# Kernel tuning notes

Hardware: AMD Instinct MI355X
Metric: run time of the kernel (lower is better)

Reference implementation:

```python
import jax, jax.numpy as jnp
import numpy as np

B, T, D = 1, 2048, 1024
H, S, LV = 16, 64, 12   # heads, state_size, num_levels = ceil(log2(T)) + 1
HD = D // H             # head_dim = 64
NEG = -1e30


def _level_matrix(length, num_levels):
    """Hierarchical level of key s w.r.t. query t (level_base=2, WEAK htype).

    level(t,s) = 0 if s == t, else floor(log2(s XOR t)) + 1, which is exactly the
    size-class of the Fenwick/dyadic segment of the prefix [0,t) containing s.
    Computed as the count of powers 2^k <= (s XOR t) to avoid float log.
    """
    t = np.arange(length)
    xor = t[:, None] ^ t[None, :]
    lv = np.zeros((length, length), dtype=np.int32)
    for k in range(num_levels - 1):
        lv += (xor >= (1 << k)).astype(np.int32)
    return jnp.asarray(lv)  # [T, T]


def _forward(x, Wq, Wk, Wv, Wdl, Wdt, Wout, A_log, dt_bias, Lp, ln_g, ln_b):
    Bb, Tt, Dd = x.shape
    Q = (x @ Wq.T).reshape(Bb, Tt, H, S)
    K = (x @ Wk.T).reshape(Bb, Tt, H, S)
    V = (x @ Wv.T).reshape(Bb, Tt, H, HD)
    dl = (x @ Wdl.T).reshape(Bb, Tt, H, LV)

    A = -jnp.exp(A_log)                                  # [H]
    dt = jax.nn.softplus(x @ Wdt.T + dt_bias)            # [B,T,H]
    g = A[None, None, :] * dt                            # [B,T,H]  (negative)
    Lam = jax.nn.softplus(Lp[None, None] * dl)           # [B,T,H,LV] lambda per level

    # Mamba2/SSD decay: M[t,s] = exp(sum_{i=s+1..t} g_i), causal
    cg = jnp.cumsum(g, axis=1)                           # [B,T,H]
    diff = cg[:, :, None, :] - cg[:, None, :, :]         # [B,T,S,H]
    tri = np.tril(np.ones((Tt, Tt), dtype=bool))
    decay = jnp.exp(jnp.where(tri[None, :, :, None], diff, NEG))  # [B,T,S,H]

    # hierarchical lambda gate: lam_ts[b,t,h,s] = Lam[b,t,h, level(t,s)]
    levels = _level_matrix(Tt, LV)                       # [T,S] int32
    lam_ts = jnp.take_along_axis(
        Lam[:, :, :, None, :], levels[None, :, None, :, None], axis=-1
    )[..., 0]                                            # [B,T,H,S]

    scores = jnp.einsum('bthd,bshd->bhts', Q, K) * (S ** -0.5)   # [B,H,T,S]
    Wmat = scores * jnp.transpose(decay, (0, 3, 1, 2)) * jnp.transpose(lam_ts, (0, 2, 1, 3))
    Y = jnp.einsum('bhts,bshd->bthd', Wmat, V).reshape(Bb, Tt, H * HD)

    o = Y @ Wout.T + x                                   # out_proj + residual
    mu = o.mean(-1, keepdims=True)
    var = ((o - mu) ** 2).mean(-1, keepdims=True)
    return (o - mu) * jax.lax.rsqrt(var + 1e-5) * ln_g + ln_b


def setup_inputs() -> dict:
    ks = jax.random.split(jax.random.key(0), 8)
    n = jax.random.normal
    w = 0.02
    return {
        'x': n(ks[0], (B, T, D), jnp.float32),
        'Wq': n(ks[1], (H * S, D), jnp.float32) * w,
        'Wk': n(ks[2], (H * S, D), jnp.float32) * w,
        'Wv': n(ks[3], (H * HD, D), jnp.float32) * w,
        'Wdl': n(ks[4], (H * LV, D), jnp.float32) * w,
        'Wdt': n(ks[5], (H, D), jnp.float32) * w,
        'Wout': n(ks[6], (D, H * HD), jnp.float32) * w,
        'A_log': jnp.log(jnp.arange(1, H + 1, dtype=jnp.float32)),
        'dt_bias': n(ks[7], (H,), jnp.float32),
        'Lp': jnp.ones((H, LV), jnp.float32),
        'ln_g': jnp.ones((D,), jnp.float32),
        'ln_b': jnp.zeros((D,), jnp.float32),
    }


def reference(x, Wq, Wk, Wv, Wdl, Wdt, Wout, A_log, dt_bias, Lp, ln_g, ln_b):
    return _forward(x, Wq, Wk, Wv, Wdl, Wdt, Wout, A_log, dt_bias, Lp, ln_g, ln_b)
```

## Files before the change

### kernel.cpp

```cpp
#include <hip/hip_runtime.h>
#include <math.h>

#define Tn 2048
#define Dn 1024
#define Hn 16
#define Sn 64
#define LVn 12
#define HDn 64
#define NQKV 3328

typedef short short8 __attribute__((ext_vector_type(8)));
typedef unsigned short ushortv8 __attribute__((ext_vector_type(8)));
typedef float floatx4 __attribute__((ext_vector_type(4)));

__device__ __forceinline__ float softplus_f(float z) {
  return (z > 0.f) ? (z + log1pf(expf(-z))) : log1pf(expf(z));
}

__device__ __forceinline__ unsigned short f2bf(float f) {
  union { float f; unsigned u; } v; v.f = f;
  unsigned r = v.u + 0x7FFF + ((v.u >> 16) & 1);
  return (unsigned short)(r >> 16);
}

__device__ __forceinline__ void cvt8(const float* s, unsigned short* d) {
  const float4 u0 = *(const float4*)s;
  const float4 u1 = *(const float4*)(s + 4);
  ushortv8 o;
  o[0] = f2bf(u0.x); o[1] = f2bf(u0.y); o[2] = f2bf(u0.z); o[3] = f2bf(u0.w);
  o[4] = f2bf(u1.x); o[5] = f2bf(u1.y); o[6] = f2bf(u1.z); o[7] = f2bf(u1.w);
  *(ushortv8*)d = o;
}

__device__ __forceinline__ void gld16(const void* g, void* l) {
  __builtin_amdgcn_global_load_lds(
      (const __attribute__((address_space(1))) unsigned int*)g,
      (__attribute__((address_space(3))) unsigned int*)l, 16, 0, 0);
}

__global__ __launch_bounds__(256) void cvtdt_k(
    const float* __restrict__ x, const float* __restrict__ Wq,
    const float* __restrict__ Wk, const float* __restrict__ Wv,
    const float* __restrict__ Wdl, const float* __restrict__ Wout,
    const float* __restrict__ Wdt, const float* __restrict__ A_log,
    const float* __restrict__ dt_bias,
    unsigned short* __restrict__ xb, unsigned short* __restrict__ wcat,
    unsigned short* __restrict__ wob, float* __restrict__ g) {
  const int chunk = blockIdx.x;
  const int tid = threadIdx.x;
  if (chunk < 3200) {
    const int eo = tid * 8;
    if (chunk < 1024) {
      const int e = chunk * 2048 + eo;
      cvt8(&x[e], &xb[e]);
    } else if (chunk < 2688) {
      const int e = (chunk - 1024) * 2048 + eo;
      const int row = e >> 10, col = e & 1023;
      if (row < 1024)       cvt8(&Wq[(size_t)row * 1024 + col], &wcat[e]);
      else if (row < 2048)  cvt8(&Wk[(size_t)(row - 1024) * 1024 + col], &wcat[e]);
      else if (row < 3072)  cvt8(&Wv[(size_t)(row - 2048) * 1024 + col], &wcat[e]);
      else if (row < 3264)  cvt8(&Wdl[(size_t)(row - 3072) * 1024 + col], &wcat[e]);
      else                  *(ushortv8*)&wcat[e] = (ushortv8)0;
    } else {
      const int e = (chunk - 2688) * 2048 + eo;
      cvt8(&Wout[e], &wob[e]);
    }
  } else {
    const int t = chunk - 3200;
    __shared__ float xs[Dn];
    ((float4*)xs)[tid] = ((const float4*)&x[(size_t)t * Dn])[tid];
    __syncthreads();
    const int h = tid >> 4, j = tid & 15;
    const float4* xr = (const float4*)&xs[j * 64];
    const float4* wr = (const float4*)&Wdt[h * Dn + j * 64];
    float acc = 0.f;
#pragma unroll
    for (int u = 0; u < 16; ++u) {
      const int up = (u + j) & 15;
      const float4 a = xr[up], b = wr[up];
      acc += a.x * b.x + a.y * b.y + a.z * b.z + a.w * b.w;
    }
#pragma unroll
    for (int st = 1; st < 16; st <<= 1) acc += __shfl_xor(acc, st);
    if (j == 0) {
      const float dtv = softplus_f(acc + dt_bias[h]);
      g[t * Hn + h] = -expf(A_log[h]) * dtv;
    }
  }
}

__global__ __launch_bounds__(256) void mfma_gemm_k(
    const unsigned short* __restrict__ A, const unsigned short* __restrict__ B,
    unsigned short* __restrict__ Cb, float* __restrict__ Cf,
    int by_scan, const float* __restrict__ g, double* __restrict__ cg) {
  __shared__ __attribute__((aligned(16))) unsigned short pool[32768];
  const int tid = threadIdx.x;
  if ((int)blockIdx.y == by_scan) {
    const int h = blockIdx.x;
    if (h >= Hn) return;
    double* ls = (double*)pool;
    double v[8];
    double run = 0.0;
#pragma unroll
    for (int i = 0; i < 8; ++i) {
      run += (double)g[(tid * 8 + i) * Hn + h];
      v[i] = run;
    }
    ls[tid] = run;
    __syncthreads();
    for (int off = 1; off < 256; off <<= 1) {
      double add = (tid >= off) ? ls[tid - off] : 0.0;
      __syncthreads();
      ls[tid] += add;
      __syncthreads();
    }
    const double excl = ls[tid] - run;
#pragma unroll
    for (int i = 0; i < 8; ++i) cg[(tid * 8 + i) * Hn + h] = excl + v[i];
    return;
  }
  unsigned short* lA = pool;
  unsigned short* lB = pool + 16384;
  const int bm = blockIdx.x * 128, bn = blockIdx.y * 128;
  const int lane = tid & 63, wave = tid >> 6;
  const int wm = wave >> 1, wn = wave & 1;
  const int l16 = lane & 15, lk = lane >> 4;
  const int sr = tid >> 2, sc = (tid & 3) * 8;
  floatx4 acc[4][4] = {};
  for (int k0 = 0; k0 < Dn; k0 += 128) {
    __syncthreads();
#pragma unroll
    for (int q = 0; q < 4; ++q) {
      gld16(&A[(size_t)(bm + sr) * Dn + k0 + q * 32 + sc],      &lA[q * 4096 + tid * 8]);
      gld16(&A[(size_t)(bm + 64 + sr) * Dn + k0 + q * 32 + sc], &lA[q * 4096 + 2048 + tid * 8]);
      gld16(&B[(size_t)(bn + sr) * Dn + k0 + q * 32 + sc],      &lB[q * 4096 + tid * 8]);
      gld16(&B[(size_t)(bn + 64 + sr) * Dn + k0 + q * 32 + sc], &lB[q * 4096 + 2048 + tid * 8]);
    }
    __syncthreads();
#pragma unroll
    for (int hh = 0; hh < 4; ++hh) {
      short8 a[4], b[4];
#pragma unroll
      for (int mf = 0; mf < 4; ++mf)
        a[mf] = *(const short8*)&lA[hh * 4096 + (wm * 64 + mf * 16 + l16) * 32 + lk * 8];
#pragma unroll
      for (int nf = 0; nf < 4; ++nf)
        b[nf] = *(const short8*)&lB[hh * 4096 + (wn * 64 + nf * 16 + l16) * 32 + lk * 8];
#pragma unroll
      for (int mf = 0; mf < 4; ++mf)
#pragma unroll
        for (int nf = 0; nf < 4; ++nf)
          acc[mf][nf] = __builtin_amdgcn_mfma_f32_16x16x32_bf16(
              a[mf], b[nf], acc[mf][nf], 0, 0, 0);
    }
  }
  if (bn < 3072) {
    unsigned short (*ctile)[136] = (unsigned short(*)[136])pool;
#pragma unroll
    for (int hh = 0; hh < 2; ++hh) {
      __syncthreads();
      if (wm == hh) {
#pragma unroll
        for (int mf = 0; mf < 4; ++mf)
#pragma unroll
          for (int nf = 0; nf < 4; ++nf)
#pragma unroll
            for (int r = 0; r < 4; ++r)
              ctile[mf * 16 + lk * 4 + r][wn * 64 + nf * 16 + l16] =
                  f2bf(acc[mf][nf][r]);
      }
      __syncthreads();
      const int rr = tid >> 4, cc = (tid & 15) * 8;
#pragma unroll
      for (int j = 0; j < 4; ++j) {
        const int row = rr + j * 16;
        *(ushortv8*)&Cb[(size_t)(bm + hh * 64 + row) * 3072 + bn + cc] =
            *(const ushortv8*)&ctile[row][cc];
      }
    }
    return;
  }
#pragma unroll
  for (int mf = 0; mf < 4; ++mf) {
#pragma unroll
    for (int nf = 0; nf < 4; ++nf) {
      const int col = bn + wn * 64 + nf * 16 + l16;
#pragma unroll
      for (int r = 0; r < 4; ++r) {
        const int row = bm + wm * 64 + mf * 16 + lk * 4 + r;
        Cf[(size_t)row * 256 + (col - 3072)] = acc[mf][nf][r];
      }
    }
  }
}

__global__ __launch_bounds__(256) void attn_k(
    const unsigned short* __restrict__ QKV, const double* __restrict__ cg,
    const float* __restrict__ dlb, const float* __restrict__ Lp,
    unsigned short* __restrict__ Y) {
  const int h = blockIdx.y;
  const int t0 = blockIdx.x * 64;
  __shared__ unsigned short Qs[64][72], Ks[64][72], Ps[64][72], Vt[64][72];
  __shared__ float cgT[64], cgS[64];
  __shared__ float lamT[64][LVn];
  const int tid = threadIdx.x;
  const int lane = tid & 63, wave = tid >> 6;
  const int wm = wave >> 1, wn = wave & 1;
  const int l16 = lane & 15, lk = lane >> 4;
  const unsigned short* Q = QKV + h * Sn;
  const unsigned short* K = QKV + 1024 + h * Sn;
  const unsigned short* V = QKV + 2048 + h * HDn;

#pragma unroll
  for (int p = 0; p < 2; ++p) {
    const int c = tid + p * 256, r = c >> 3, c8 = (c & 7) * 8;
    *(ushortv8*)&Qs[r][c8] = *(const ushortv8*)&Q[(size_t)(t0 + r) * 3072 + c8];
  }
  if (tid < 64) cgT[tid] = (float)cg[(t0 + tid) * Hn + h];
  for (int i = tid; i < 64 * LVn; i += 256) {
    const int r = i / LVn, l = i % LVn;
    lamT[r][l] = softplus_f(Lp[h * LVn + l] * dlb[(size_t)(t0 + r) * 256 + h * LVn + l]);
  }

  floatx4 accY[2][2] = {};

  for (int s0 = t0; s0 >= 0; s0 -= 64) {
    __syncthreads();
#pragma unroll
    for (int p = 0; p < 2; ++p) {
      const int c = tid + p * 256, r = c >> 3, c8 = (c & 7) * 8;
      *(ushortv8*)&Ks[r][c8] = *(const ushortv8*)&K[(size_t)(s0 + r) * 3072 + c8];
      const ushortv8 vv = *(const ushortv8*)&V[(size_t)(s0 + r) * 3072 + c8];
#pragma unroll
      for (int j = 0; j < 8; ++j) {
        const int dd = c8 + j;
        Vt[dd][((((r >> 3) ^ (dd >> 3)) & 7) << 3) | (r & 7)] = vv[j];
      }
    }
    if (tid < 64) cgS[tid] = (float)cg[(s0 + tid) * Hn + h];
    __syncthreads();

    if (s0 + 64 <= t0 && cgT[0] - cgS[63] < -80.f) break;

    floatx4 sc[2][2] = {};
    __builtin_amdgcn_s_setprio(1);
#pragma unroll
    for (int kk = 0; kk < 2; ++kk) {
      short8 aq0 = *(const short8*)&Qs[(wm * 2 + 0) * 16 + l16][kk * 32 + lk * 8];
      short8 aq1 = *(const short8*)&Qs[(wm * 2 + 1) * 16 + l16][kk * 32 + lk * 8];
      short8 bk0 = *(const short8*)&Ks[(wn * 2 + 0) * 16 + l16][kk * 32 + lk * 8];
      short8 bk1 = *(const short8*)&Ks[(wn * 2 + 1) * 16 + l16][kk * 32 + lk * 8];
      sc[0][0] = __builtin_amdgcn_mfma_f32_16x16x32_bf16(aq0, bk0, sc[0][0], 0, 0, 0);
      sc[0][1] = __builtin_amdgcn_mfma_f32_16x16x32_bf16(aq0, bk1, sc[0][1], 0, 0, 0);
      sc[1][0] = __builtin_amdgcn_mfma_f32_16x16x32_bf16(aq1, bk0, sc[1][0], 0, 0, 0);
      sc[1][1] = __builtin_amdgcn_mfma_f32_16x16x32_bf16(aq1, bk1, sc[1][1], 0, 0, 0);
    }
    __builtin_amdgcn_s_setprio(0);

#pragma unroll
    for (int mi = 0; mi < 2; ++mi) {
#pragma unroll
      for (int ni = 0; ni < 2; ++ni) {
        const int s_loc = (wn * 2 + ni) * 16 + l16;
        const int s_g = s0 + s_loc;
        const float cs = cgS[s_loc];
#pragma unroll
        for (int r = 0; r < 4; ++r) {
          const int t_loc = (wm * 2 + mi) * 16 + lk * 4 + r;
          const int t_g = t0 + t_loc;
          float val = 0.f;
          if (s_g <= t_g) {
            const float dd = cgT[t_loc] - cs;
            const int xr = t_g ^ s_g;
            const int lvl = xr ? (32 - __clz(xr)) : 0;
            val = sc[mi][ni][r] * 0.125f * __expf(dd) * lamT[t_loc][lvl];
          }
          Ps[t_loc][s_loc] = f2bf(val);
        }
      }
    }
    __syncthreads();

    __builtin_amdgcn_s_setprio(1);
#pragma unroll
    for (int kk = 0; kk < 2; ++kk) {
      short8 ap0 = *(const short8*)&Ps[(wm * 2 + 0) * 16 + l16][kk * 32 + lk * 8];
      short8 ap1 = *(const short8*)&Ps[(wm * 2 + 1) * 16 + l16][kk * 32 + lk * 8];
      const int d0 = (wn * 2 + 0) * 16 + l16;
      const int d1 = (wn * 2 + 1) * 16 + l16;
      short8 bv0 = *(const short8*)&Vt[d0][(((kk * 4 + lk) ^ (d0 >> 3)) & 7) << 3];
      short8 bv1 = *(const short8*)&Vt[d1][(((kk * 4 + lk) ^ (d1 >> 3)) & 7) << 3];
      accY[0][0] = __builtin_amdgcn_mfma_f32_16x16x32_bf16(ap0, bv0, accY[0][0], 0, 0, 0);
      accY[0][1] = __builtin_amdgcn_mfma_f32_16x16x32_bf16(ap0, bv1, accY[0][1], 0, 0, 0);
      accY[1][0] = __builtin_amdgcn_mfma_f32_16x16x32_bf16(ap1, bv0, accY[1][0], 0, 0, 0);
      accY[1][1] = __builtin_amdgcn_mfma_f32_16x16x32_bf16(ap1, bv1, accY[1][1], 0, 0, 0);
    }
    __builtin_amdgcn_s_setprio(0);
  }

  __syncthreads();
#pragma unroll
  for (int mi = 0; mi < 2; ++mi)
#pragma unroll
    for (int ni = 0; ni < 2; ++ni)
#pragma unroll
      for (int r = 0; r < 4; ++r)
        Ps[(wm * 2 + mi) * 16 + lk * 4 + r][(wn * 2 + ni) * 16 + l16] =
            f2bf(accY[mi][ni][r]);
  __syncthreads();
#pragma unroll
  for (int p = 0; p < 2; ++p) {
    const int c = tid + p * 256, r = c >> 3, c8 = (c & 7) * 8;
    *(ushortv8*)&Y[(size_t)(t0 + r) * Dn + h * HDn + c8] = *(const ushortv8*)&Ps[r][c8];
  }
}

__global__ __launch_bounds__(256) void outproj_k(
    const unsigned short* __restrict__ A, const unsigned short* __restrict__ B,
    const float* __restrict__ R, float* __restrict__ out) {
  __shared__ unsigned short lA[4 * 64 * 32];
  __shared__ unsigned short lB[4 * 64 * 32];
  const int tid = threadIdx.x;
  const int bm = blockIdx.x * 64, bn = blockIdx.y * 64;
  const int lane = tid & 63, wave = tid >> 6;
  const int wm = wave >> 1, wn = wave & 1;
  const int l16 = lane & 15, lk = lane >> 4;
  const int sr = tid >> 2, sc = (tid & 3) * 8;
  floatx4 acc[2][2] = {};
  for (int k0 = 0; k0 < Dn; k0 += 128) {
    __syncthreads();
#pragma unroll
    for (int q = 0; q < 4; ++q) {
      gld16(&A[(size_t)(bm + sr) * Dn + k0 + q * 32 + sc], &lA[q * 2048 + tid * 8]);
      gld16(&B[(size_t)(bn + sr) * Dn + k0 + q * 32 + sc], &lB[q * 2048 + tid * 8]);
    }
    __syncthreads();
#pragma unroll
    for (int hh = 0; hh < 4; ++hh) {
      short8 a[2], b[2];
#pragma unroll
      for (int mf = 0; mf < 2; ++mf)
        a[mf] = *(const short8*)&lA[hh * 2048 + (wm * 32 + mf * 16 + l16) * 32 + lk * 8];
#pragma unroll
      for (int nf = 0; nf < 2; ++nf)
        b[nf] = *(const short8*)&lB[hh * 2048 + (wn * 32 + nf * 16 + l16) * 32 + lk * 8];
#pragma unroll
      for (int mf = 0; mf < 2; ++mf)
#pragma unroll
        for (int nf = 0; nf < 2; ++nf)
          acc[mf][nf] = __builtin_amdgcn_mfma_f32_16x16x32_bf16(
              a[mf], b[nf], acc[mf][nf], 0, 0, 0);
    }
  }
#pragma unroll
  for (int mf = 0; mf < 2; ++mf) {
#pragma unroll
    for (int nf = 0; nf < 2; ++nf) {
      const int col = bn + wn * 32 + nf * 16 + l16;
#pragma unroll
      for (int r = 0; r < 4; ++r) {
        const int row = bm + wm * 32 + mf * 16 + lk * 4 + r;
        out[(size_t)row * Dn + col] =
            acc[mf][nf][r] + R[(size_t)row * Dn + col];
      }
    }
  }
}

__global__ __launch_bounds__(256) void ln_k(float* __restrict__ io,
                                            const float* __restrict__ gw,
                                            const float* __restrict__ bw) {
  const int t = blockIdx.x;
  const int tid = threadIdx.x;
  const float4 v = ((const float4*)(io + t * Dn))[tid];
  float s = v.x + v.y + v.z + v.w;
  float q = v.x * v.x + v.y * v.y + v.z * v.z + v.w * v.w;
#pragma unroll
  for (int off = 32; off >= 1; off >>= 1) {
    s += __shfl_down(s, off);
    q += __shfl_down(q, off);
  }
  __shared__ float sm[4], qm[4];
  const int w = tid >> 6, lane = tid & 63;
  if (lane == 0) { sm[w] = s; qm[w] = q; }
  __syncthreads();
  const float S_ = sm[0] + sm[1] + sm[2] + sm[3];
  const float Q_ = qm[0] + qm[1] + qm[2] + qm[3];
  const float mu = S_ * (1.f / Dn);
  const float var = Q_ * (1.f / Dn) - mu * mu;
  const float inv = rsqrtf(var + 1e-5f);
  const float4 gg = ((const float4*)gw)[tid];
  const float4 bb = ((const float4*)bw)[tid];
  float4 o;
  o.x = (v.x - mu) * inv * gg.x + bb.x;
  o.y = (v.y - mu) * inv * gg.y + bb.y;
  o.z = (v.z - mu) * inv * gg.z + bb.z;
  o.w = (v.w - mu) * inv * gg.w + bb.w;
  ((float4*)(io + t * Dn))[tid] = o;
}

extern "C" void kernel_launch(void* const* d_in, const int* in_sizes, int n_in,
                              void* d_out, int out_size, void* d_ws, size_t ws_size,
                              hipStream_t stream) {
  (void)in_sizes; (void)n_in; (void)out_size; (void)ws_size;
  const float* x      = (const float*)d_in[0];
  const float* Wq     = (const float*)d_in[1];
  const float* Wk     = (const float*)d_in[2];
  const float* Wv     = (const float*)d_in[3];
  const float* Wdl    = (const float*)d_in[4];
  const float* Wdt    = (const float*)d_in[5];
  const float* Wout   = (const float*)d_in[6];
  const float* A_log  = (const float*)d_in[7];
  const float* dt_bias= (const float*)d_in[8];
  const float* Lp     = (const float*)d_in[9];
  const float* ln_g   = (const float*)d_in[10];
  const float* ln_b   = (const float*)d_in[11];
  float* out = (float*)d_out;
  float* ws  = (float*)d_ws;

  const size_t MAT = (size_t)Tn * Dn;
  const size_t WSZ = (size_t)Dn * Dn;
  size_t off = 0;
  float*  gb   = ws + off; off += (size_t)Tn * Hn;
  double* cgd  = (double*)(ws + off); off += 2 * (size_t)Tn * Hn;
  float*  dlb  = ws + off; off += (size_t)Tn * 256;
  unsigned short* xb16  = (unsigned short*)(ws + off); off += MAT / 2;
  unsigned short* Wcat16= (unsigned short*)(ws + off); off += (size_t)NQKV * Dn / 2;
  unsigned short* Wo16  = (unsigned short*)(ws + off); off += WSZ / 2;
  unsigned short* QKV16 = (unsigned short*)(ws + off); off += (size_t)Tn * 3072 / 2;
  unsigned short* Y16   = (unsigned short*)(ws + off); off += MAT / 2;

  cvtdt_k<<<dim3(5248), 256, 0, stream>>>(x, Wq, Wk, Wv, Wdl, Wout, Wdt,
                                          A_log, dt_bias, xb16, Wcat16, Wo16, gb);
  mfma_gemm_k<<<dim3(Tn / 128, NQKV / 128 + 1), 256, 0, stream>>>(
      xb16, Wcat16, QKV16, dlb, NQKV / 128, gb, cgd);
  attn_k<<<dim3(Tn / 64, Hn), 256, 0, stream>>>(QKV16, cgd, dlb, Lp, Y16);
  outproj_k<<<dim3(Tn / 64, Dn / 64), 256, 0, stream>>>(Y16, Wo16, x, out);
  ln_k<<<dim3(Tn), 256, 0, stream>>>(out, ln_g, ln_b);
}
```

Before: 86.00 us.

## Fuse all stages into one persistent kernel with software grid barriers

Replaces the five separate launches (convert/dt, QKV GEMM plus scan, attention, out-projection, layernorm) with a single persistent 512-block kernel. The stages are separated by atomic-counter grid barriers, plus a tiny init kernel that resets the counters. This removes per-launch overhead and the tail gaps between kernels. In exchange, each stage now runs on a fixed block count with no overlap, the barriers spin-wait, and correctness depends on all 512 blocks being co-resident.

```diff
diff --git a/kernel.cpp b/kernel.cpp
--- a/kernel.cpp
+++ b/kernel.cpp
@@ -8,6 +8,7 @@
 #define LVn 12
 #define HDn 64
 #define NQKV 3328
+#define NBLK 512
 
 typedef short short8 __attribute__((ext_vector_type(8)));
 typedef unsigned short ushortv8 __attribute__((ext_vector_type(8)));
@@ -38,72 +39,164 @@
       (__attribute__((address_space(3))) unsigned int*)l, 16, 0, 0);
 }
 
-__global__ __launch_bounds__(256) void cvtdt_k(
-    const float* __restrict__ x, const float* __restrict__ Wq,
-    const float* __restrict__ Wk, const float* __restrict__ Wv,
-    const float* __restrict__ Wdl, const float* __restrict__ Wout,
-    const float* __restrict__ Wdt, const float* __restrict__ A_log,
-    const float* __restrict__ dt_bias,
-    unsigned short* __restrict__ xb, unsigned short* __restrict__ wcat,
-    unsigned short* __restrict__ wob, float* __restrict__ g) {
-  const int chunk = blockIdx.x;
+__device__ __forceinline__ void gridbar(unsigned* ctr, int idx) {
+  __syncthreads();
+  if (threadIdx.x == 0) {
+    __threadfence();
+    unsigned arrived = atomicAdd(&ctr[idx], 1u) + 1;
+    if (arrived < NBLK) {
+      while (__hip_atomic_load(&ctr[idx], __ATOMIC_RELAXED,
+                               __HIP_MEMORY_SCOPE_AGENT) < NBLK)
+        __builtin_amdgcn_s_sleep(10);
+    }
+    __threadfence();
+  }
+  __syncthreads();
+}
+
+__global__ void init_k(unsigned* ctr) {
+  if (threadIdx.x < 8) ctr[threadIdx.x] = 0;
+}
+
+struct MegaP {
+  const float *x, *Wq, *Wk, *Wv, *Wdl, *Wout, *Wdt, *A_log, *dt_bias, *Lp,
+              *ln_g, *ln_b;
+  float *out, *gb, *dlb;
+  double *cgd;
+  unsigned short *xb16, *Wcat16, *Wo16, *QKV16, *Y16;
+  unsigned *ctr;
+};
+
+__global__ __launch_bounds__(256, 2) void mega_k(MegaP P) {
+  __shared__ __attribute__((aligned(16))) unsigned char smem[65536];
+  const int bid = blockIdx.x;
   const int tid = threadIdx.x;
-  if (chunk < 3200) {
-    const int eo = tid * 8;
-    if (chunk < 1024) {
-      const int e = chunk * 2048 + eo;
-      cvt8(&x[e], &xb[e]);
-    } else if (chunk < 2688) {
-      const int e = (chunk - 1024) * 2048 + eo;
-      const int row = e >> 10, col = e & 1023;
-      if (row < 1024)       cvt8(&Wq[(size_t)row * 1024 + col], &wcat[e]);
-      else if (row < 2048)  cvt8(&Wk[(size_t)(row - 1024) * 1024 + col], &wcat[e]);
-      else if (row < 3072)  cvt8(&Wv[(size_t)(row - 2048) * 1024 + col], &wcat[e]);
-      else if (row < 3264)  cvt8(&Wdl[(size_t)(row - 3072) * 1024 + col], &wcat[e]);
-      else                  *(ushortv8*)&wcat[e] = (ushortv8)0;
+
+  for (int chunk = bid; chunk < 5248; chunk += NBLK) {
+    if (chunk < 3200) {
+      const int eo = tid * 8;
+      if (chunk < 1024) {
+        const int e = chunk * 2048 + eo;
+        cvt8(&P.x[e], &P.xb16[e]);
+      } else if (chunk < 2688) {
+        const int e = (chunk - 1024) * 2048 + eo;
+        const int row = e >> 10, col = e & 1023;
+        if (row < 1024)       cvt8(&P.Wq[(size_t)row * 1024 + col], &P.Wcat16[e]);
+        else if (row < 2048)  cvt8(&P.Wk[(size_t)(row - 1024) * 1024 + col], &P.Wcat16[e]);
+        else if (row < 3072)  cvt8(&P.Wv[(size_t)(row - 2048) * 1024 + col], &P.Wcat16[e]);
+        else if (row < 3264)  cvt8(&P.Wdl[(size_t)(row - 3072) * 1024 + col], &P.Wcat16[e]);
+        else                  *(ushortv8*)&P.Wcat16[e] = (ushortv8)0;
+      } else {
+        const int e = (chunk - 2688) * 2048 + eo;
+        cvt8(&P.Wout[e], &P.Wo16[e]);
+      }
     } else {
-      const int e = (chunk - 2688) * 2048 + eo;
-      cvt8(&Wout[e], &wob[e]);
-    }
-  } else {
-    const int t = chunk - 3200;
-    __shared__ float xs[Dn];
-    ((float4*)xs)[tid] = ((const float4*)&x[(size_t)t * Dn])[tid];
-    __syncthreads();
-    const int h = tid >> 4, j = tid & 15;
-    const float4* xr = (const float4*)&xs[j * 64];
-    const float4* wr = (const float4*)&Wdt[h * Dn + j * 64];
-    float acc = 0.f;
-#pragma unroll
-    for (int u = 0; u < 16; ++u) {
-      const int up = (u + j) & 15;
-      const float4 a = xr[up], b = wr[up];
-      acc += a.x * b.x + a.y * b.y + a.z * b.z + a.w * b.w;
-    }
-#pragma unroll
-    for (int st = 1; st < 16; st <<= 1) acc += __shfl_xor(acc, st);
-    if (j == 0) {
-      const float dtv = softplus_f(acc + dt_bias[h]);
-      g[t * Hn + h] = -expf(A_log[h]) * dtv;
-    }
-  }
-}
-
-__global__ __launch_bounds__(256) void mfma_gemm_k(
-    const unsigned short* __restrict__ A, const unsigned short* __restrict__ B,
-    unsigned short* __restrict__ Cb, float* __restrict__ Cf,
-    int by_scan, const float* __restrict__ g, double* __restrict__ cg) {
-  __shared__ __attribute__((aligned(16))) unsigned short pool[32768];
-  const int tid = threadIdx.x;
-  if ((int)blockIdx.y == by_scan) {
-    const int h = blockIdx.x;
-    if (h >= Hn) return;
-    double* ls = (double*)pool;
+      const int t = chunk - 3200;
+      float* xs = (float*)smem;
+      ((float4*)xs)[tid] = ((const float4*)&P.x[(size_t)t * Dn])[tid];
+      __syncthreads();
+      const int h = tid >> 4, j = tid & 15;
+      const float4* xr = (const float4*)&xs[j * 64];
+      const float4* wr = (const float4*)&P.Wdt[h * Dn + j * 64];
+      float acc = 0.f;
+#pragma unroll
+      for (int u = 0; u < 16; ++u) {
+        const int up = (u + j) & 15;
+        const float4 a = xr[up], b = wr[up];
+        acc += a.x * b.x + a.y * b.y + a.z * b.z + a.w * b.w;
+      }
+#pragma unroll
+      for (int st = 1; st < 16; st <<= 1) acc += __shfl_xor(acc, st);
+      if (j == 0) {
+        const float dtv = softplus_f(acc + P.dt_bias[h]);
+        P.gb[t * Hn + h] = -expf(P.A_log[h]) * dtv;
+      }
+      __syncthreads();
+    }
+  }
+  gridbar(P.ctr, 0);
+
+  if (bid < 416) {
+    unsigned short* lA = (unsigned short*)smem;
+    unsigned short* lB = lA + 16384;
+    const int bm = (bid & 15) * 128, bn = (bid >> 4) * 128;
+    const int lane = tid & 63, wave = tid >> 6;
+    const int wm = wave >> 1, wn = wave & 1;
+    const int l16 = lane & 15, lk = lane >> 4;
+    const int sr = tid >> 2, sc = (tid & 3) * 8;
+    floatx4 acc[4][4] = {};
+    for (int k0 = 0; k0 < Dn; k0 += 128) {
+      __syncthreads();
+#pragma unroll
+      for (int q = 0; q < 4; ++q) {
+        gld16(&P.xb16[(size_t)(bm + sr) * Dn + k0 + q * 32 + sc],      &lA[q * 4096 + tid * 8]);
+        gld16(&P.xb16[(size_t)(bm + 64 + sr) * Dn + k0 + q * 32 + sc], &lA[q * 4096 + 2048 + tid * 8]);
+        gld16(&P.Wcat16[(size_t)(bn + sr) * Dn + k0 + q * 32 + sc],      &lB[q * 4096 + tid * 8]);
+        gld16(&P.Wcat16[(size_t)(bn + 64 + sr) * Dn + k0 + q * 32 + sc], &lB[q * 4096 + 2048 + tid * 8]);
+      }
+      __syncthreads();
+#pragma unroll
+      for (int hh = 0; hh < 4; ++hh) {
+        short8 a[4], b[4];
+#pragma unroll
+        for (int mf = 0; mf < 4; ++mf)
+          a[mf] = *(const short8*)&lA[hh * 4096 + (wm * 64 + mf * 16 + l16) * 32 + lk * 8];
+#pragma unroll
+        for (int nf = 0; nf < 4; ++nf)
+          b[nf] = *(const short8*)&lB[hh * 4096 + (wn * 64 + nf * 16 + l16) * 32 + lk * 8];
+#pragma unroll
+        for (int mf = 0; mf < 4; ++mf)
+#pragma unroll
+          for (int nf = 0; nf < 4; ++nf)
+            acc[mf][nf] = __builtin_amdgcn_mfma_f32_16x16x32_bf16(
+                a[mf], b[nf], acc[mf][nf], 0, 0, 0);
+      }
+    }
+    if (bn < 3072) {
+      unsigned short (*ctile)[136] = (unsigned short(*)[136])smem;
+#pragma unroll
+      for (int hh = 0; hh < 2; ++hh) {
+        __syncthreads();
+        if (wm == hh) {
+#pragma unroll
+          for (int mf = 0; mf < 4; ++mf)
+#pragma unroll
+            for (int nf = 0; nf < 4; ++nf)
+#pragma unroll
+              for (int r = 0; r < 4; ++r)
+                ctile[mf * 16 + lk * 4 + r][wn * 64 + nf * 16 + l16] =
+                    f2bf(acc[mf][nf][r]);
+        }
+        __syncthreads();
+        const int rr = tid >> 4, cc = (tid & 15) * 8;
+#pragma unroll
+        for (int j = 0; j < 4; ++j) {
+          const int row = rr + j * 16;
+          *(ushortv8*)&P.QKV16[(size_t)(bm + hh * 64 + row) * 3072 + bn + cc] =
+              *(const ushortv8*)&ctile[row][cc];
+        }
+      }
+    } else {
+#pragma unroll
+      for (int mf = 0; mf < 4; ++mf)
+#pragma unroll
+        for (int nf = 0; nf < 4; ++nf) {
+          const int col = bn + wn * 64 + nf * 16 + l16;
+#pragma unroll
+          for (int r = 0; r < 4; ++r) {
+            const int row = bm + wm * 64 + mf * 16 + lk * 4 + r;
+            P.dlb[(size_t)row * 256 + (col - 3072)] = acc[mf][nf][r];
+          }
+        }
+    }
+  } else if (bid < 432) {
+    const int h = bid - 416;
+    double* ls = (double*)smem;
     double v[8];
     double run = 0.0;
 #pragma unroll
     for (int i = 0; i < 8; ++i) {
-      run += (double)g[(tid * 8 + i) * Hn + h];
+      run += (double)P.gb[(tid * 8 + i) * Hn + h];
       v[i] = run;
     }
     ls[tid] = run;
@@ -116,287 +209,212 @@
     }
     const double excl = ls[tid] - run;
 #pragma unroll
-    for (int i = 0; i < 8; ++i) cg[(tid * 8 + i) * Hn + h] = excl + v[i];
-    return;
-  }
-  unsigned short* lA = pool;
-  unsigned short* lB = pool + 16384;
-  const int bm = blockIdx.x * 128, bn = blockIdx.y * 128;
-  const int lane = tid & 63, wave = tid >> 6;
-  const int wm = wave >> 1, wn = wave & 1;
-  const int l16 = lane & 15, lk = lane >> 4;
-  const int sr = tid >> 2, sc = (tid & 3) * 8;
-  floatx4 acc[4][4] = {};
-  for (int k0 = 0; k0 < Dn; k0 += 128) {
-    __syncthreads();
-#pragma unroll
-    for (int q = 0; q < 4; ++q) {
-      gld16(&A[(size_t)(bm + sr) * Dn + k0 + q * 32 + sc],      &lA[q * 4096 + tid * 8]);
-      gld16(&A[(size_t)(bm + 64 + sr) * Dn + k0 + q * 32 + sc], &lA[q * 4096 + 2048 + tid * 8]);
-      gld16(&B[(size_t)(bn + sr) * Dn + k0 + q * 32 + sc],      &lB[q * 4096 + tid * 8]);
-      gld16(&B[(size_t)(bn + 64 + sr) * Dn + k0 + q * 32 + sc], &lB[q * 4096 + 2048 + tid * 8]);
-    }
-    __syncthreads();
-#pragma unroll
-    for (int hh = 0; hh < 4; ++hh) {
-      short8 a[4], b[4];
-#pragma unroll
-      for (int mf = 0; mf < 4; ++mf)
-        a[mf] = *(const short8*)&lA[hh * 4096 + (wm * 64 + mf * 16 + l16) * 32 + lk * 8];
-#pragma unroll
-      for (int nf = 0; nf < 4; ++nf)
-        b[nf] = *(const short8*)&lB[hh * 4096 + (wn * 64 + nf * 16 + l16) * 32 + lk * 8];
-#pragma unroll
-      for (int mf = 0; mf < 4; ++mf)
-#pragma unroll
-        for (int nf = 0; nf < 4; ++nf)
-          acc[mf][nf] = __builtin_amdgcn_mfma_f32_16x16x32_bf16(
-              a[mf], b[nf], acc[mf][nf], 0, 0, 0);
-    }
-  }
-  if (bn < 3072) {
-    unsigned short (*ctile)[136] = (unsigned short(*)[136])pool;
-#pragma unroll
-    for (int hh = 0; hh < 2; ++hh) {
-      __syncthreads();
-      if (wm == hh) {
-#pragma unroll
-        for (int mf = 0; mf < 4; ++mf)
-#pragma unroll
-          for (int nf = 0; nf < 4; ++nf)
-#pragma unroll
-            for (int r = 0; r < 4; ++r)
-              ctile[mf * 16 + lk * 4 + r][wn * 64 + nf * 16 + l16] =
-                  f2bf(acc[mf][nf][r]);
-      }
-      __syncthreads();
-      const int rr = tid >> 4, cc = (tid & 15) * 8;
-#pragma unroll
-      for (int j = 0; j < 4; ++j) {
-        const int row = rr + j * 16;
-        *(ushortv8*)&Cb[(size_t)(bm + hh * 64 + row) * 3072 + bn + cc] =
-            *(const ushortv8*)&ctile[row][cc];
-      }
-    }
-    return;
-  }
-#pragma unroll
-  for (int mf = 0; mf < 4; ++mf) {
-#pragma unroll
-    for (int nf = 0; nf < 4; ++nf) {
-      const int col = bn + wn * 64 + nf * 16 + l16;
-#pragma unroll
-      for (int r = 0; r < 4; ++r) {
-        const int row = bm + wm * 64 + mf * 16 + lk * 4 + r;
-        Cf[(size_t)row * 256 + (col - 3072)] = acc[mf][nf][r];
-      }
-    }
-  }
-}
-
-__global__ __launch_bounds__(256) void attn_k(
-    const unsigned short* __restrict__ QKV, const double* __restrict__ cg,
-    const float* __restrict__ dlb, const float* __restrict__ Lp,
-    unsigned short* __restrict__ Y) {
-  const int h = blockIdx.y;
-  const int t0 = blockIdx.x * 64;
-  __shared__ unsigned short Qs[64][72], Ks[64][72], Ps[64][72], Vt[64][72];
-  __shared__ float cgT[64], cgS[64];
-  __shared__ float lamT[64][LVn];
-  const int tid = threadIdx.x;
-  const int lane = tid & 63, wave = tid >> 6;
-  const int wm = wave >> 1, wn = wave & 1;
-  const int l16 = lane & 15, lk = lane >> 4;
-  const unsigned short* Q = QKV + h * Sn;
-  const unsigned short* K = QKV + 1024 + h * Sn;
-  const unsigned short* V = QKV + 2048 + h * HDn;
-
-#pragma unroll
-  for (int p = 0; p < 2; ++p) {
-    const int c = tid + p * 256, r = c >> 3, c8 = (c & 7) * 8;
-    *(ushortv8*)&Qs[r][c8] = *(const ushortv8*)&Q[(size_t)(t0 + r) * 3072 + c8];
-  }
-  if (tid < 64) cgT[tid] = (float)cg[(t0 + tid) * Hn + h];
-  for (int i = tid; i < 64 * LVn; i += 256) {
-    const int r = i / LVn, l = i % LVn;
-    lamT[r][l] = softplus_f(Lp[h * LVn + l] * dlb[(size_t)(t0 + r) * 256 + h * LVn + l]);
-  }
-
-  floatx4 accY[2][2] = {};
-
-  for (int s0 = t0; s0 >= 0; s0 -= 64) {
-    __syncthreads();
+    for (int i = 0; i < 8; ++i) P.cgd[(tid * 8 + i) * Hn + h] = excl + v[i];
+  }
+  gridbar(P.ctr, 1);
+
+  {
+    const int h = bid >> 5;
+    const int t0 = (bid & 31) * 64;
+    unsigned short (*Qs)[72] = (unsigned short (*)[72])smem;
+    unsigned short (*Ks)[72] = (unsigned short (*)[72])(smem + 9216);
+    unsigned short (*Ps)[72] = (unsigned short (*)[72])(smem + 18432);
+    unsigned short (*Vt)[72] = (unsigned short (*)[72])(smem + 27648);
+    float* cgT = (float*)(smem + 36864);
+    float* cgS = (float*)(smem + 37120);
+    float (*lamT)[LVn] = (float (*)[LVn])(smem + 37376);
+    const int lane = tid & 63, wave = tid >> 6;
+    const int wm = wave >> 1, wn = wave & 1;
+    const int l16 = lane & 15, lk = lane >> 4;
+    const unsigned short* Q = P.QKV16 + h * Sn;
+    const unsigned short* K = P.QKV16 + 1024 + h * Sn;
+    const unsigned short* V = P.QKV16 + 2048 + h * HDn;
+
 #pragma unroll
     for (int p = 0; p < 2; ++p) {
       const int c = tid + p * 256, r = c >> 3, c8 = (c & 7) * 8;
-      *(ushortv8*)&Ks[r][c8] = *(const ushortv8*)&K[(size_t)(s0 + r) * 3072 + c8];
-      const ushortv8 vv = *(const ushortv8*)&V[(size_t)(s0 + r) * 3072 + c8];
-#pragma unroll
-      for (int j = 0; j < 8; ++j) {
-        const int dd = c8 + j;
-        Vt[dd][((((r >> 3) ^ (dd >> 3)) & 7) << 3) | (r & 7)] = vv[j];
-      }
-    }
-    if (tid < 64) cgS[tid] = (float)cg[(s0 + tid) * Hn + h];
+      *(ushortv8*)&Qs[r][c8] = *(const ushortv8*)&Q[(size_t)(t0 + r) * 3072 + c8];
+    }
+    if (tid < 64) cgT[tid] = (float)P.cgd[(t0 + tid) * Hn + h];
+    for (int i = tid; i < 64 * LVn; i += 256) {
+      const int r = i / LVn, l = i % LVn;
+      lamT[r][l] = softplus_f(
+          P.Lp[h * LVn + l] * P.dlb[(size_t)(t0 + r) * 256 + h * LVn + l]);
+    }
+
+    floatx4 accY[2][2] = {};
+
+    for (int s0 = t0; s0 >= 0; s0 -= 64) {
+      __syncthreads();
+#pragma unroll
+      for (int p = 0; p < 2; ++p) {
+        const int c = tid + p * 256, r = c >> 3, c8 = (c & 7) * 8;
+        *(ushortv8*)&Ks[r][c8] = *(const ushortv8*)&K[(size_t)(s0 + r) * 3072 + c8];
+        const ushortv8 vv = *(const ushortv8*)&V[(size_t)(s0 + r) * 3072 + c8];
+#pragma unroll
+        for (int j = 0; j < 8; ++j) {
+          const int dd = c8 + j;
+          Vt[dd][((((r >> 3) ^ (dd >> 3)) & 7) << 3) | (r & 7)] = vv[j];
+        }
+      }
+      if (tid < 64) cgS[tid] = (float)P.cgd[(s0 + tid) * Hn + h];
+      __syncthreads();
+
+      if (s0 + 64 <= t0 && cgT[0] - cgS[63] < -80.f) break;
+
+      floatx4 sc[2][2] = {};
+      __builtin_amdgcn_s_setprio(1);
+#pragma unroll
+      for (int kk = 0; kk < 2; ++kk) {
+        short8 aq0 = *(const short8*)&Qs[(wm * 2 + 0) * 16 + l16][kk * 32 + lk * 8];
+        short8 aq1 = *(const short8*)&Qs[(wm * 2 + 1) * 16 + l16][kk * 32 + lk * 8];
+        short8 bk0 = *(const short8*)&Ks[(wn * 2 + 0) * 16 + l16][kk * 32 + lk * 8];
+        short8 bk1 = *(const short8*)&Ks[(wn * 2 + 1) * 16 + l16][kk * 32 + lk * 8];
+        sc[0][0] = __builtin_amdgcn_mfma_f32_16x16x32_bf16(aq0, bk0, sc[0][0], 0, 0, 0);
+        sc[0][1] = __builtin_amdgcn_mfma_f32_16x16x32_bf16(aq0, bk1, sc[0][1], 0, 0, 0);
+        sc[1][0] = __builtin_amdgcn_mfma_f32_16x16x32_bf16(aq1, bk0, sc[1][0], 0, 0, 0);
+        sc[1][1] = __builtin_amdgcn_mfma_f32_16x16x32_bf16(aq1, bk1, sc[1][1], 0, 0, 0);
+      }
+      __builtin_amdgcn_s_setprio(0);
+
+#pragma unroll
+      for (int mi = 0; mi < 2; ++mi) {
+#pragma unroll
+        for (int ni = 0; ni < 2; ++ni) {
+          const int s_loc = (wn * 2 + ni) * 16 + l16;
+          const int s_g = s0 + s_loc;
+          const float cs = cgS[s_loc];
+#pragma unroll
+          for (int r = 0; r < 4; ++r) {
+            const int t_loc = (wm * 2 + mi) * 16 + lk * 4 + r;
+            const int t_g = t0 + t_loc;
+            float val = 0.f;
+            if (s_g <= t_g) {
+              const float dd = cgT[t_loc] - cs;
+              const int xr = t_g ^ s_g;
+              const int lvl = xr ? (32 - __clz(xr)) : 0;
+              val = sc[mi][ni][r] * 0.125f * __expf(dd) * lamT[t_loc][lvl];
+            }
+            Ps[t_loc][s_loc] = f2bf(val);
+          }
+        }
+      }
+      __syncthreads();
+
+      __builtin_amdgcn_s_setprio(1);
+#pragma unroll
+      for (int kk = 0; kk < 2; ++kk) {
+        short8 ap0 = *(const short8*)&Ps[(wm * 2 + 0) * 16 + l16][kk * 32 + lk * 8];
+        short8 ap1 = *(const short8*)&Ps[(wm * 2 + 1) * 16 + l16][kk * 32 + lk * 8];
+        const int d0 = (wn * 2 + 0) * 16 + l16;
+        const int d1 = (wn * 2 + 1) * 16 + l16;
+        short8 bv0 = *(const short8*)&Vt[d0][(((kk * 4 + lk) ^ (d0 >> 3)) & 7) << 3];
+        short8 bv1 = *(const short8*)&Vt[d1][(((kk * 4 + lk) ^ (d1 >> 3)) & 7) << 3];
+        accY[0][0] = __builtin_amdgcn_mfma_f32_16x16x32_bf16(ap0, bv0, accY[0][0], 0, 0, 0);
+        accY[0][1] = __builtin_amdgcn_mfma_f32_16x16x32_bf16(ap0, bv1, accY[0][1], 0, 0, 0);
+        accY[1][0] = __builtin_amdgcn_mfma_f32_16x16x32_bf16(ap1, bv0, accY[1][0], 0, 0, 0);
+        accY[1][1] = __builtin_amdgcn_mfma_f32_16x16x32_bf16(ap1, bv1, accY[1][1], 0, 0, 0);
+      }
+      __builtin_amdgcn_s_setprio(0);
+    }
+
     __syncthreads();
-
-    if (s0 + 64 <= t0 && cgT[0] - cgS[63] < -80.f) break;
-
-    floatx4 sc[2][2] = {};
-    __builtin_amdgcn_s_setprio(1);
-#pragma unroll
-    for (int kk = 0; kk < 2; ++kk) {
-      short8 aq0 = *(const short8*)&Qs[(wm * 2 + 0) * 16 + l16][kk * 32 + lk * 8];
-      short8 aq1 = *(const short8*)&Qs[(wm * 2 + 1) * 16 + l16][kk * 32 + lk * 8];
-      short8 bk0 = *(const short8*)&Ks[(wn * 2 + 0) * 16 + l16][kk * 32 + lk * 8];
-      short8 bk1 = *(const short8*)&Ks[(wn * 2 + 1) * 16 + l16][kk * 32 + lk * 8];
-      sc[0][0] = __builtin_amdgcn_mfma_f32_16x16x32_bf16(aq0, bk0, sc[0][0], 0, 0, 0);
-      sc[0][1] = __builtin_amdgcn_mfma_f32_16x16x32_bf16(aq0, bk1, sc[0][1], 0, 0, 0);
-      sc[1][0] = __builtin_amdgcn_mfma_f32_16x16x32_bf16(aq1, bk0, sc[1][0], 0, 0, 0);
-      sc[1][1] = __builtin_amdgcn_mfma_f32_16x16x32_bf16(aq1, bk1, sc[1][1], 0, 0, 0);
-    }
-    __builtin_amdgcn_s_setprio(0);
-
-#pragma unroll
-    for (int mi = 0; mi < 2; ++mi) {
-#pragma unroll
-      for (int ni = 0; ni < 2; ++ni) {
-        const int s_loc = (wn * 2 + ni) * 16 + l16;
-        const int s_g = s0 + s_loc;
-        const float cs = cgS[s_loc];
+#pragma unroll
+    for (int mi = 0; mi < 2; ++mi)
+#pragma unroll
+      for (int ni = 0; ni < 2; ++ni)
+#pragma unroll
+        for (int r = 0; r < 4; ++r)
+          Ps[(wm * 2 + mi) * 16 + lk * 4 + r][(wn * 2 + ni) * 16 + l16] =
+              f2bf(accY[mi][ni][r]);
+    __syncthreads();
+#pragma unroll
+    for (int p = 0; p < 2; ++p) {
+      const int c = tid + p * 256, r = c >> 3, c8 = (c & 7) * 8;
+      *(ushortv8*)&P.Y16[(size_t)(t0 + r) * Dn + h * HDn + c8] =
+          *(const ushortv8*)&Ps[r][c8];
+    }
+  }
+  gridbar(P.ctr, 2);
+
+  {
+    unsigned short* lA = (unsigned short*)smem;
+    unsigned short* lB = lA + 8192;
+    const int bm = (bid & 31) * 64, bn = (bid >> 5) * 64;
+    const int lane = tid & 63, wave = tid >> 6;
+    const int wm = wave >> 1, wn = wave & 1;
+    const int l16 = lane & 15, lk = lane >> 4;
+    const int sr = tid >> 2, sc = (tid & 3) * 8;
+    floatx4 acc[2][2] = {};
+    for (int k0 = 0; k0 < Dn; k0 += 128) {
+      __syncthreads();
+#pragma unroll
+      for (int q = 0; q < 4; ++q) {
+        gld16(&P.Y16[(size_t)(bm + sr) * Dn + k0 + q * 32 + sc], &lA[q * 2048 + tid * 8]);
+        gld16(&P.Wo16[(size_t)(bn + sr) * Dn + k0 + q * 32 + sc], &lB[q * 2048 + tid * 8]);
+      }
+      __syncthreads();
+#pragma unroll
+      for (int hh = 0; hh < 4; ++hh) {
+        short8 a[2], b[2];
+#pragma unroll
+        for (int mf = 0; mf < 2; ++mf)
+          a[mf] = *(const short8*)&lA[hh * 2048 + (wm * 32 + mf * 16 + l16) * 32 + lk * 8];
+#pragma unroll
+        for (int nf = 0; nf < 2; ++nf)
+          b[nf] = *(const short8*)&lB[hh * 2048 + (wn * 32 + nf * 16 + l16) * 32 + lk * 8];
+#pragma unroll
+        for (int mf = 0; mf < 2; ++mf)
+#pragma unroll
+          for (int nf = 0; nf < 2; ++nf)
+            acc[mf][nf] = __builtin_amdgcn_mfma_f32_16x16x32_bf16(
+                a[mf], b[nf], acc[mf][nf], 0, 0, 0);
+      }
+    }
+#pragma unroll
+    for (int mf = 0; mf < 2; ++mf)
+#pragma unroll
+      for (int nf = 0; nf < 2; ++nf) {
+        const int col = bn + wn * 32 + nf * 16 + l16;
 #pragma unroll
         for (int r = 0; r < 4; ++r) {
-          const int t_loc = (wm * 2 + mi) * 16 + lk * 4 + r;
-          const int t_g = t0 + t_loc;
-          float val = 0.f;
-          if (s_g <= t_g) {
-            const float dd = cgT[t_loc] - cs;
-            const int xr = t_g ^ s_g;
-            const int lvl = xr ? (32 - __clz(xr)) : 0;
-            val = sc[mi][ni][r] * 0.125f * __expf(dd) * lamT[t_loc][lvl];
-          }
-          Ps[t_loc][s_loc] = f2bf(val);
-        }
-      }
-    }
+          const int row = bm + wm * 32 + mf * 16 + lk * 4 + r;
+          P.out[(size_t)row * Dn + col] =
+              acc[mf][nf][r] + P.x[(size_t)row * Dn + col];
+        }
+      }
+  }
+  gridbar(P.ctr, 3);
+
+  for (int t = bid; t < Tn; t += NBLK) {
+    float* sm = (float*)smem;
+    float* qm = sm + 4;
+    const float4 v = ((const float4*)(P.out + (size_t)t * Dn))[tid];
+    float s = v.x + v.y + v.z + v.w;
+    float q = v.x * v.x + v.y * v.y + v.z * v.z + v.w * v.w;
+#pragma unroll
+    for (int off = 32; off >= 1; off >>= 1) {
+      s += __shfl_down(s, off);
+      q += __shfl_down(q, off);
+    }
+    const int w = tid >> 6, lane = tid & 63;
+    if (lane == 0) { sm[w] = s; qm[w] = q; }
     __syncthreads();
-
-    __builtin_amdgcn_s_setprio(1);
-#pragma unroll
-    for (int kk = 0; kk < 2; ++kk) {
-      short8 ap0 = *(const short8*)&Ps[(wm * 2 + 0) * 16 + l16][kk * 32 + lk * 8];
-      short8 ap1 = *(const short8*)&Ps[(wm * 2 + 1) * 16 + l16][kk * 32 + lk * 8];
-      const int d0 = (wn * 2 + 0) * 16 + l16;
-      const int d1 = (wn * 2 + 1) * 16 + l16;
-      short8 bv0 = *(const short8*)&Vt[d0][(((kk * 4 + lk) ^ (d0 >> 3)) & 7) << 3];
-      short8 bv1 = *(const short8*)&Vt[d1][(((kk * 4 + lk) ^ (d1 >> 3)) & 7) << 3];
-      accY[0][0] = __builtin_amdgcn_mfma_f32_16x16x32_bf16(ap0, bv0, accY[0][0], 0, 0, 0);
-      accY[0][1] = __builtin_amdgcn_mfma_f32_16x16x32_bf16(ap0, bv1, accY[0][1], 0, 0, 0);
-      accY[1][0] = __builtin_amdgcn_mfma_f32_16x16x32_bf16(ap1, bv0, accY[1][0], 0, 0, 0);
-      accY[1][1] = __builtin_amdgcn_mfma_f32_16x16x32_bf16(ap1, bv1, accY[1][1], 0, 0, 0);
-    }
-    __builtin_amdgcn_s_setprio(0);
-  }
-
-  __syncthreads();
-#pragma unroll
-  for (int mi = 0; mi < 2; ++mi)
-#pragma unroll
-    for (int ni = 0; ni < 2; ++ni)
-#pragma unroll
-      for (int r = 0; r < 4; ++r)
-        Ps[(wm * 2 + mi) * 16 + lk * 4 + r][(wn * 2 + ni) * 16 + l16] =
-            f2bf(accY[mi][ni][r]);
-  __syncthreads();
-#pragma unroll
-  for (int p = 0; p < 2; ++p) {
-    const int c = tid + p * 256, r = c >> 3, c8 = (c & 7) * 8;
-    *(ushortv8*)&Y[(size_t)(t0 + r) * Dn + h * HDn + c8] = *(const ushortv8*)&Ps[r][c8];
-  }
-}
-
-__global__ __launch_bounds__(256) void outproj_k(
-    const unsigned short* __restrict__ A, const unsigned short* __restrict__ B,
-    const float* __restrict__ R, float* __restrict__ out) {
-  __shared__ unsigned short lA[4 * 64 * 32];
-  __shared__ unsigned short lB[4 * 64 * 32];
-  const int tid = threadIdx.x;
-  const int bm = blockIdx.x * 64, bn = blockIdx.y * 64;
-  const int lane = tid & 63, wave = tid >> 6;
-  const int wm = wave >> 1, wn = wave & 1;
-  const int l16 = lane & 15, lk = lane >> 4;
-  const int sr = tid >> 2, sc = (tid & 3) * 8;
-  floatx4 acc[2][2] = {};
-  for (int k0 = 0; k0 < Dn; k0 += 128) {
+    const float S_ = sm[0] + sm[1] + sm[2] + sm[3];
+    const float Q_ = qm[0] + qm[1] + qm[2] + qm[3];
+    const float mu = S_ * (1.f / Dn);
+    const float var = Q_ * (1.f / Dn) - mu * mu;
+    const float inv = rsqrtf(var + 1e-5f);
+    const float4 gg = ((const float4*)P.ln_g)[tid];
+    const float4 bb = ((const float4*)P.ln_b)[tid];
+    float4 o;
+    o.x = (v.x - mu) * inv * gg.x + bb.x;
+    o.y = (v.y - mu) * inv * gg.y + bb.y;
+    o.z = (v.z - mu) * inv * gg.z + bb.z;
+    o.w = (v.w - mu) * inv * gg.w + bb.w;
+    ((float4*)(P.out + (size_t)t * Dn))[tid] = o;
     __syncthreads();
-#pragma unroll
-    for (int q = 0; q < 4; ++q) {
-      gld16(&A[(size_t)(bm + sr) * Dn + k0 + q * 32 + sc], &lA[q * 2048 + tid * 8]);
-      gld16(&B[(size_t)(bn + sr) * Dn + k0 + q * 32 + sc], &lB[q * 2048 + tid * 8]);
-    }
-    __syncthreads();
-#pragma unroll
-    for (int hh = 0; hh < 4; ++hh) {
-      short8 a[2], b[2];
-#pragma unroll
-      for (int mf = 0; mf < 2; ++mf)
-        a[mf] = *(const short8*)&lA[hh * 2048 + (wm * 32 + mf * 16 + l16) * 32 + lk * 8];
-#pragma unroll
-      for (int nf = 0; nf < 2; ++nf)
-        b[nf] = *(const short8*)&lB[hh * 2048 + (wn * 32 + nf * 16 + l16) * 32 + lk * 8];
-#pragma unroll
-      for (int mf = 0; mf < 2; ++mf)
-#pragma unroll
-        for (int nf = 0; nf < 2; ++nf)
-          acc[mf][nf] = __builtin_amdgcn_mfma_f32_16x16x32_bf16(
-              a[mf], b[nf], acc[mf][nf], 0, 0, 0);
-    }
-  }
-#pragma unroll
-  for (int mf = 0; mf < 2; ++mf) {
-#pragma unroll
-    for (int nf = 0; nf < 2; ++nf) {
-      const int col = bn + wn * 32 + nf * 16 + l16;
-#pragma unroll
-      for (int r = 0; r < 4; ++r) {
-        const int row = bm + wm * 32 + mf * 16 + lk * 4 + r;
-        out[(size_t)row * Dn + col] =
-            acc[mf][nf][r] + R[(size_t)row * Dn + col];
-      }
-    }
-  }
-}
-
-__global__ __launch_bounds__(256) void ln_k(float* __restrict__ io,
-                                            const float* __restrict__ gw,
-                                            const float* __restrict__ bw) {
-  const int t = blockIdx.x;
-  const int tid = threadIdx.x;
-  const float4 v = ((const float4*)(io + t * Dn))[tid];
-  float s = v.x + v.y + v.z + v.w;
-  float q = v.x * v.x + v.y * v.y + v.z * v.z + v.w * v.w;
-#pragma unroll
-  for (int off = 32; off >= 1; off >>= 1) {
-    s += __shfl_down(s, off);
-    q += __shfl_down(q, off);
-  }
-  __shared__ float sm[4], qm[4];
-  const int w = tid >> 6, lane = tid & 63;
-  if (lane == 0) { sm[w] = s; qm[w] = q; }
-  __syncthreads();
-  const float S_ = sm[0] + sm[1] + sm[2] + sm[3];
-  const float Q_ = qm[0] + qm[1] + qm[2] + qm[3];
-  const float mu = S_ * (1.f / Dn);
-  const float var = Q_ * (1.f / Dn) - mu * mu;
-  const float inv = rsqrtf(var + 1e-5f);
-  const float4 gg = ((const float4*)gw)[tid];
-  const float4 bb = ((const float4*)bw)[tid];
-  float4 o;
-  o.x = (v.x - mu) * inv * gg.x + bb.x;
-  o.y = (v.y - mu) * inv * gg.y + bb.y;
-  o.z = (v.z - mu) * inv * gg.z + bb.z;
-  o.w = (v.w - mu) * inv * gg.w + bb.w;
-  ((float4*)(io + t * Dn))[tid] = o;
+  }
 }
 
 extern "C" void kernel_launch(void* const* d_in, const int* in_sizes, int n_in,
@@ -424,17 +442,21 @@
   float*  gb   = ws + off; off += (size_t)Tn * Hn;
   double* cgd  = (double*)(ws + off); off += 2 * (size_t)Tn * Hn;
   float*  dlb  = ws + off; off += (size_t)Tn * 256;
+  unsigned* ctr = (unsigned*)(ws + off); off += 8;
   unsigned short* xb16  = (unsigned short*)(ws + off); off += MAT / 2;
   unsigned short* Wcat16= (unsigned short*)(ws + off); off += (size_t)NQKV * Dn / 2;
   unsigned short* Wo16  = (unsigned short*)(ws + off); off += WSZ / 2;
   unsigned short* QKV16 = (unsigned short*)(ws + off); off += (size_t)Tn * 3072 / 2;
   unsigned short* Y16   = (unsigned short*)(ws + off); off += MAT / 2;
 
-  cvtdt_k<<<dim3(5248), 256, 0, stream>>>(x, Wq, Wk, Wv, Wdl, Wout, Wdt,
-                                          A_log, dt_bias, xb16, Wcat16, Wo16, gb);
-  mfma_gemm_k<<<dim3(Tn / 128, NQKV / 128 + 1), 256, 0, stream>>>(
-      xb16, Wcat16, QKV16, dlb, NQKV / 128, gb, cgd);
-  attn_k<<<dim3(Tn / 64, Hn), 256, 0, stream>>>(QKV16, cgd, dlb, Lp, Y16);
-  outproj_k<<<dim3(Tn / 64, Dn / 64), 256, 0, stream>>>(Y16, Wo16, x, out);
-  ln_k<<<dim3(Tn), 256, 0, stream>>>(out, ln_g, ln_b);
-}
+  MegaP P;
+  P.x = x; P.Wq = Wq; P.Wk = Wk; P.Wv = Wv; P.Wdl = Wdl; P.Wout = Wout;
+  P.Wdt = Wdt; P.A_log = A_log; P.dt_bias = dt_bias; P.Lp = Lp;
+  P.ln_g = ln_g; P.ln_b = ln_b;
+  P.out = out; P.gb = gb; P.dlb = dlb; P.cgd = cgd;
+  P.xb16 = xb16; P.Wcat16 = Wcat16; P.Wo16 = Wo16; P.QKV16 = QKV16; P.Y16 = Y16;
+  P.ctr = ctr;
+
+  init_k<<<dim3(1), 32, 0, stream>>>(ctr);
+  mega_k<<<dim3(NBLK), 256, 0, stream>>>(P);
+}
```

Result: slower. 297.3 us (+245.7%).
